# Optimization experiments

Measured on AMD Instinct MI355X. Metric: run time of the kernel, lower is better.

The kernel has to match this reference:

```python
import jax, jax.numpy as jnp
import numpy as np

DIM = 2048
HEADS = 16
DIM_HEAD = 128
DIM_INNER = HEADS * DIM_HEAD
BATCH = 2
SEQ = 2048
EPS = 1e-12  # F.normalize default eps


def l2norm(t, axis=-1):
    # matches F.normalize(t, dim=axis, p=2): t / max(||t||, eps)
    n = jnp.sqrt(jnp.sum(t * t, axis=axis, keepdims=True))
    return t / jnp.maximum(n, EPS)


def setup_inputs() -> dict:
    key = jax.random.key(0)
    ks = jax.random.split(key, 5)
    x = jax.random.normal(ks[0], (BATCH, SEQ, DIM), dtype=jnp.float32)
    # NormLinear weights (torch Linear layout: [out, in]); parametrization
    # l2-normalizes rows (dim=-1) for q/k/v and columns (dim=0) for to_out.
    Wq = jax.random.normal(ks[1], (DIM_INNER, DIM), dtype=jnp.float32) / np.sqrt(DIM)
    Wk = jax.random.normal(ks[2], (DIM_INNER, DIM), dtype=jnp.float32) / np.sqrt(DIM)
    Wv = jax.random.normal(ks[3], (DIM_INNER, DIM), dtype=jnp.float32) / np.sqrt(DIM)
    Wout = jax.random.normal(ks[4], (DIM, DIM_INNER), dtype=jnp.float32) / np.sqrt(DIM_INNER)
    # Scale(dim_inner, init=1.0, scale=dim**-1): param = ones * dim**-1,
    # forward_scale = init/scale = dim, so qk_scale() starts at 1.0
    qk_scale = jnp.ones((DIM_INNER,), dtype=jnp.float32) / DIM
    return {"x": x, "Wq": Wq, "Wk": Wk, "Wv": Wv, "Wout": Wout, "qk_scale": qk_scale}


def reference(x, Wq, Wk, Wv, Wout, qk_scale):
    b, n, _ = x.shape
    # NormLinear: x @ l2norm(W, rows).T  (scale = groups**-1 = 1)
    q = jnp.einsum('bnd,ed->bne', x, l2norm(Wq, axis=-1))
    k = jnp.einsum('bnd,ed->bne', x, l2norm(Wk, axis=-1))
    v = jnp.einsum('bnd,ed->bne', x, l2norm(Wv, axis=-1))
    # split heads: b n (h d) -> b h n d
    split = lambda t: t.reshape(b, n, HEADS, DIM_HEAD).transpose(0, 2, 1, 3)
    q, k, v = split(q), split(k), split(v)
    # per-head l2norm of q and k over head dim
    q = l2norm(q, axis=-1)
    k = l2norm(k, axis=-1)
    # learned qk scale: (h d) -> h 1 d, effective = param * forward_scale(=DIM)
    q = q * (qk_scale * DIM).reshape(HEADS, 1, DIM_HEAD)
    # causal SDPA with scale = sqrt(dim_head) (unit-norm q,k in nGPT)
    attn_scale = DIM_HEAD ** 0.5
    scores = jnp.einsum('bhid,bhjd->bhij', q, k) * attn_scale
    causal = jnp.tril(jnp.ones((n, n), dtype=bool))
    scores = jnp.where(causal, scores, jnp.finfo(scores.dtype).min)
    attn = jax.nn.softmax(scores, axis=-1)
    out = jnp.einsum('bhij,bhjd->bhid', attn, v)
    # merge heads: b h n d -> b n (h d)
    out = out.transpose(0, 2, 1, 3).reshape(b, n, DIM_INNER)
    # to_out: NormLinear with norm over dim=0 of weight [DIM, DIM_INNER]
    out = jnp.einsum('bne,de->bnd', out, l2norm(Wout, axis=0))
    return out
```

## Files before the change

### kernel.cpp

```cpp
#include <hip/hip_runtime.h>


typedef __bf16 bf16x8 __attribute__((ext_vector_type(8)));
typedef float f32x4 __attribute__((ext_vector_type(4)));

__device__ __forceinline__ unsigned short f2bf(float f) {
  unsigned int u = __float_as_uint(f);
  u = u + 0x7FFFu + ((u >> 16) & 1u);
  return (unsigned short)(u >> 16);
}

__device__ __forceinline__ void async16(const void* g, void* l) {
  __builtin_amdgcn_global_load_lds(
      (const __attribute__((address_space(1))) unsigned int*)g,
      (__attribute__((address_space(3))) unsigned int*)l, 16, 0, 0);
}

#define QFOLD (2048.0f * 11.313708498984761f * 1.4426950408889634f)


__global__ __launch_bounds__(256) void prep_w_rows(
    const float* __restrict__ Wq, const float* __restrict__ Wk,
    const float* __restrict__ Wv, ushort* __restrict__ oq,
    ushort* __restrict__ ok_, ushort* __restrict__ ov) {
  const int row = blockIdx.x;
  const float* W = (blockIdx.y == 0) ? Wq : (blockIdx.y == 1) ? Wk : Wv;
  ushort* O = (blockIdx.y == 0) ? oq : (blockIdx.y == 1) ? ok_ : ov;
  const int t = threadIdx.x;
  const float4* Wr = (const float4*)(W + (size_t)row * 2048);
  float4 v0 = Wr[t];
  float4 v1 = Wr[t + 256];
  float ss = v0.x * v0.x + v0.y * v0.y + v0.z * v0.z + v0.w * v0.w +
             v1.x * v1.x + v1.y * v1.y + v1.z * v1.z + v1.w * v1.w;
  ss += __shfl_xor(ss, 1);  ss += __shfl_xor(ss, 2);
  ss += __shfl_xor(ss, 4);  ss += __shfl_xor(ss, 8);
  ss += __shfl_xor(ss, 16); ss += __shfl_xor(ss, 32);
  __shared__ float red[4];
  if ((t & 63) == 0) red[t >> 6] = ss;
  __syncthreads();
  float tot = red[0] + red[1] + red[2] + red[3];
  float sc = 1.0f / fmaxf(sqrtf(tot), 1e-12f);
  ushort4 o0, o1;
  o0.x = f2bf(v0.x * sc); o0.y = f2bf(v0.y * sc);
  o0.z = f2bf(v0.z * sc); o0.w = f2bf(v0.w * sc);
  o1.x = f2bf(v1.x * sc); o1.y = f2bf(v1.y * sc);
  o1.z = f2bf(v1.z * sc); o1.w = f2bf(v1.w * sc);
  *(ushort4*)(O + (size_t)row * 2048 + t * 4) = o0;
  *(ushort4*)(O + (size_t)row * 2048 + 1024 + t * 4) = o1;
}

__global__ __launch_bounds__(256) void wout_colss(const float* __restrict__ W,
                                                  float* __restrict__ colss) {
  const int e = blockIdx.x * 256 + threadIdx.x;
  const int d0 = blockIdx.y * 128;
  float ss = 0.f;
  #pragma unroll 8
  for (int i = 0; i < 128; ++i) {
    float v = W[(size_t)(d0 + i) * 2048 + e];
    ss += v * v;
  }
  atomicAdd(colss + e, ss);
}

__global__ __launch_bounds__(256) void wout_norm(const float* __restrict__ W,
                                                 const float* __restrict__ colss,
                                                 ushort* __restrict__ O) {
  const int idx = (blockIdx.x * 256 + threadIdx.x) * 4;
  float4 v = *(const float4*)(W + idx);
  float4 c = *(const float4*)(colss + (idx & 2047));
  ushort4 o;
  o.x = f2bf(v.x / fmaxf(sqrtf(c.x), 1e-12f));
  o.y = f2bf(v.y / fmaxf(sqrtf(c.y), 1e-12f));
  o.z = f2bf(v.z / fmaxf(sqrtf(c.z), 1e-12f));
  o.w = f2bf(v.w / fmaxf(sqrtf(c.w), 1e-12f));
  *(ushort4*)(O + idx) = o;
}

__global__ __launch_bounds__(256) void convert_x(const float* __restrict__ X,
                                                 ushort* __restrict__ O) {
  const int idx = (blockIdx.x * 256 + threadIdx.x) * 4;
  float4 v = *(const float4*)(X + idx);
  ushort4 o;
  o.x = f2bf(v.x); o.y = f2bf(v.y); o.z = f2bf(v.z); o.w = f2bf(v.w);
  *(ushort4*)(O + idx) = o;
}

__global__ __launch_bounds__(64) void qk_mhead(const float* __restrict__ qks,
                                               float* __restrict__ mh) {
  const int h = blockIdx.x, l = threadIdx.x;
  float m = fmaxf(fabsf(qks[h * 128 + l]), fabsf(qks[h * 128 + 64 + l]));
  m = fmaxf(m, __shfl_xor(m, 1));  m = fmaxf(m, __shfl_xor(m, 2));
  m = fmaxf(m, __shfl_xor(m, 4));  m = fmaxf(m, __shfl_xor(m, 8));
  m = fmaxf(m, __shfl_xor(m, 16)); m = fmaxf(m, __shfl_xor(m, 32));
  if (l == 0) mh[h] = m * QFOLD;
}

__device__ __forceinline__ void gemm_mainloop(
    const ushort* __restrict__ A, const ushort* __restrict__ Bw,
    int m0, int n0, ushort* As, ushort* Bs, f32x4 acc[4][4],
    int t, int l, int wm, int wn) {
  const int l15 = l & 15, l4 = l >> 4;
  const ushort* abase = A + (size_t)m0 * 2048;
  const ushort* bbase = Bw + (size_t)n0 * 2048;
  for (int kt = 0; kt < 32; ++kt) {
    const int k0 = kt * 64;
    __syncthreads();
    #pragma unroll
    for (int p = 0; p < 9; ++p) {
      int c = p * 256 + t;
      const ushort* src = abase;
      char* dst = (char*)As;
      int cc = c;
      if (c >= 1152) { cc = c - 1152; src = bbase; dst = (char*)Bs; }
      int r = cc / 9, dc = cc - r * 9;
      int dcc = (dc == 8) ? 0 : dc;
      async16(src + (size_t)r * 2048 + k0 + dcc * 8, dst + cc * 16);
    }
    __syncthreads();
    #pragma unroll
    for (int ks = 0; ks < 2; ++ks) {
      bf16x8 af[4], bg[4];
      #pragma unroll
      for (int f = 0; f < 4; ++f)
        af[f] = *(const bf16x8*)&As[(wm * 64 + f * 16 + l15) * 72 + ks * 32 + l4 * 8];
      #pragma unroll
      for (int f = 0; f < 4; ++f)
        bg[f] = *(const bf16x8*)&Bs[(wn * 64 + f * 16 + l15) * 72 + ks * 32 + l4 * 8];
      #pragma unroll
      for (int fm = 0; fm < 4; ++fm)
        #pragma unroll
        for (int fn = 0; fn < 4; ++fn)
          acc[fm][fn] = __builtin_amdgcn_mfma_f32_16x16x32_bf16(
              af[fm], bg[fn], acc[fm][fn], 0, 0, 0);
    }
  }
}

__global__ __launch_bounds__(256, 4) void gemm_qkv(
    const ushort* __restrict__ X, const ushort* __restrict__ Wq,
    const ushort* __restrict__ Wk, const ushort* __restrict__ Wv,
    const float* __restrict__ qks, ushort* __restrict__ qn,
    ushort* __restrict__ kn, ushort* __restrict__ vt) {
  const int z = blockIdx.z;
  const ushort* Bw = (z == 0) ? Wq : (z == 1) ? Wk : Wv;
  const int n0 = blockIdx.x * 128;
  const int m0 = blockIdx.y * 128;
  __shared__ __align__(16) ushort As[128 * 72];
  __shared__ __align__(16) ushort Bs[128 * 72];
  __shared__ float partials[2][128];
  const int t = threadIdx.x, w = t >> 6, l = t & 63;
  const int wm = w & 1, wn = w >> 1;
  const int l15 = l & 15, l4 = l >> 4;

  f32x4 acc[4][4];
  #pragma unroll
  for (int i = 0; i < 4; ++i)
    #pragma unroll
    for (int j = 0; j < 4; ++j) acc[i][j] = (f32x4){0.f, 0.f, 0.f, 0.f};

  gemm_mainloop(X, Bw, m0, n0, As, Bs, acc, t, l, wm, wn);

  const int h = n0 >> 7;
  if (z == 2) {
    #pragma unroll
    for (int fm = 0; fm < 4; ++fm) {
      int mrow = m0 + wm * 64 + fm * 16 + l4 * 4;
      int bb = mrow >> 11;
      int nn = mrow & 2047;
      #pragma unroll
      for (int fn = 0; fn < 4; ++fn) {
        int d = wn * 64 + fn * 16 + l15;
        ushort4 p;
        p.x = f2bf(acc[fm][fn][0]); p.y = f2bf(acc[fm][fn][1]);
        p.z = f2bf(acc[fm][fn][2]); p.w = f2bf(acc[fm][fn][3]);
        *(ushort4*)(vt + (size_t)((bb * 16 + h) * 128 + d) * 2048 + nn) = p;
      }
    }
  } else {
    float rs[4][4];
    #pragma unroll
    for (int fm = 0; fm < 4; ++fm)
      #pragma unroll
      for (int r = 0; r < 4; ++r) {
        float s = 0.f;
        #pragma unroll
        for (int fn = 0; fn < 4; ++fn) {
          float v = acc[fm][fn][r];
          s += v * v;
        }
        s += __shfl_xor(s, 1); s += __shfl_xor(s, 2);
        s += __shfl_xor(s, 4); s += __shfl_xor(s, 8);
        rs[fm][r] = s;
      }
    if (l15 == 0) {
      #pragma unroll
      for (int fm = 0; fm < 4; ++fm)
        #pragma unroll
        for (int r = 0; r < 4; ++r)
          partials[wn][wm * 64 + fm * 16 + l4 * 4 + r] = rs[fm][r];
    }
    __syncthreads();
    float cs[4];
    #pragma unroll
    for (int fn = 0; fn < 4; ++fn)
      cs[fn] = (z == 0) ? qks[n0 + wn * 64 + fn * 16 + l15] * QFOLD : 1.0f;
    ushort* O = (z == 0) ? qn : kn;
    #pragma unroll
    for (int fm = 0; fm < 4; ++fm)
      #pragma unroll
      for (int r = 0; r < 4; ++r) {
        int i = wm * 64 + fm * 16 + l4 * 4 + r;
        float tot = partials[0][i] + partials[1][i];
        float sc = 1.0f / fmaxf(sqrtf(tot), 1e-12f);
        #pragma unroll
        for (int fn = 0; fn < 4; ++fn)
          O[(size_t)(m0 + i) * 2048 + n0 + wn * 64 + fn * 16 + l15] =
              f2bf(acc[fm][fn][r] * sc * cs[fn]);
      }
  }
}


#define LDSBUF 49152
#define ABYTES 32768

__device__ __forceinline__ void mainloop_256x128(
    const ushort* __restrict__ A, const ushort* __restrict__ Bw,
    int m0, int n0, char* lds, f32x4 acc[4][4], int t) {
  const int l = t & 63, w = t >> 6;
  const int wm = w & 3, wn = w >> 2;
  const int l15 = l & 15, l4 = l >> 4;

  const int lc = (t & 7) ^ ((t >> 3) & 7);
  const ushort* srcA = A + (size_t)m0 * 2048 + (t >> 3) * 2048 + lc * 8;
  const ushort* srcB = Bw + (size_t)n0 * 2048 + (t >> 3) * 2048 + lc * 8;
  char* dstA = lds + t * 16;
  char* dstB = lds + ABYTES + t * 16;

  const int rdA = (wm * 64 + l15) * 128;
  const int rdB = ABYTES + (wn * 64 + l15) * 128;
  const int cb0 = ((l4 ^ (l15 & 7)) * 16);
  const int cb1 = (((4 + l4) ^ (l15 & 7)) * 16);

  auto stageA = [&](int s, int k0, int o) {
    async16(srcA + (size_t)o * 131072 + k0, dstA + s * LDSBUF + o * 8192);
  };
  auto stageB = [&](int s, int k0, int o) {
    async16(srcB + (size_t)o * 131072 + k0, dstB + s * LDSBUF + o * 8192);
  };

  #pragma unroll
  for (int i = 0; i < 4; ++i)
    #pragma unroll
    for (int j = 0; j < 4; ++j) acc[i][j] = (f32x4){0.f, 0.f, 0.f, 0.f};

  stageA(0, 0, 0); stageA(0, 0, 1); stageA(0, 0, 2); stageA(0, 0, 3);
  stageB(0, 0, 0); stageB(0, 0, 1);
  stageA(1, 64, 0); stageA(1, 64, 1); stageA(1, 64, 2); stageA(1, 64, 3);
  stageB(1, 64, 0); stageB(1, 64, 1);
  asm volatile("s_waitcnt vmcnt(6)" ::: "memory");
  __builtin_amdgcn_s_barrier();

  auto tile = [&](int s, int s2, int k2, bool pf) {
    const char* Ab = lds + s * LDSBUF;
    bf16x8 af[4][2], bg[4][2];
    #pragma unroll
    for (int fm = 0; fm < 4; ++fm) {
      af[fm][0] = *(const bf16x8*)(Ab + rdA + fm * 2048 + cb0);
      af[fm][1] = *(const bf16x8*)(Ab + rdA + fm * 2048 + cb1);
    }
    #pragma unroll
    for (int fn = 0; fn < 2; ++fn) {
      bg[fn][0] = *(const bf16x8*)(Ab + rdB + fn * 2048 + cb0);
      bg[fn][1] = *(const bf16x8*)(Ab + rdB + fn * 2048 + cb1);
    }
    if (pf) { stageA(s2, k2, 0); stageA(s2, k2, 1); stageA(s2, k2, 2); }
    __builtin_amdgcn_s_setprio(1);
    #pragma unroll
    for (int ks = 0; ks < 2; ++ks)
      #pragma unroll
      for (int fm = 0; fm < 4; ++fm)
        #pragma unroll
        for (int fn = 0; fn < 2; ++fn)
          acc[fm][fn] = __builtin_amdgcn_mfma_f32_16x16x32_bf16(
              af[fm][ks], bg[fn][ks], acc[fm][fn], 0, 0, 0);
    __builtin_amdgcn_s_setprio(0);
    #pragma unroll
    for (int fn = 2; fn < 4; ++fn) {
      bg[fn][0] = *(const bf16x8*)(Ab + rdB + fn * 2048 + cb0);
      bg[fn][1] = *(const bf16x8*)(Ab + rdB + fn * 2048 + cb1);
    }
    if (pf) { stageA(s2, k2, 3); stageB(s2, k2, 0); stageB(s2, k2, 1); }
    __builtin_amdgcn_s_setprio(1);
    #pragma unroll
    for (int ks = 0; ks < 2; ++ks)
      #pragma unroll
      for (int fm = 0; fm < 4; ++fm)
        #pragma unroll
        for (int fn = 2; fn < 4; ++fn)
          acc[fm][fn] = __builtin_amdgcn_mfma_f32_16x16x32_bf16(
              af[fm][ks], bg[fn][ks], acc[fm][fn], 0, 0, 0);
    __builtin_amdgcn_s_setprio(0);
  };

  #pragma unroll 1
  for (int kt = 0; kt < 30; kt += 3) {
    tile(0, 2, (kt + 2) * 64, true);
    asm volatile("s_waitcnt vmcnt(6)" ::: "memory");
    __builtin_amdgcn_s_barrier();
    tile(1, 0, (kt + 3) * 64, true);
    asm volatile("s_waitcnt vmcnt(6)" ::: "memory");
    __builtin_amdgcn_s_barrier();
    tile(2, 1, (kt + 4) * 64, true);
    asm volatile("s_waitcnt vmcnt(6)" ::: "memory");
    __builtin_amdgcn_s_barrier();
  }
  tile(0, 0, 0, false);
  asm volatile("s_waitcnt vmcnt(0)" ::: "memory");
  __builtin_amdgcn_s_barrier();
  tile(1, 0, 0, false);
}

__global__ __launch_bounds__(256, 2) void attn_kernel(
    const ushort* __restrict__ qn, const ushort* __restrict__ kn,
    const ushort* __restrict__ vt, const float* __restrict__ mhead,
    ushort* __restrict__ ao) {
  const int hb = blockIdx.x;
  const int b = hb >> 4, h = hb & 15;
  const int y = blockIdx.y;
  const int qt = (y < 8) ? y : 23 - y;
  const int i0 = qt * 128;
  const int t = threadIdx.x, w = t >> 6, l = t & 63;
  const int l15 = l & 15, l4 = l >> 4;

  __shared__ __align__(16) ushort Ks[64 * 128];
  __shared__ __align__(16) ushort Vts[128 * 64];
  __shared__ __align__(16) ushort Ps[128 * 64];

  bf16x8 qf[2][4];
  #pragma unroll
  for (int fmq = 0; fmq < 2; ++fmq)
    #pragma unroll
    for (int ks = 0; ks < 4; ++ks)
      qf[fmq][ks] = *(const bf16x8*)(qn +
          (size_t)(b * 2048 + i0 + w * 32 + fmq * 16 + l15) * 2048 +
          h * 128 + ks * 32 + l4 * 8);

  f32x4 Oa[2][8];
  #pragma unroll
  for (int fmq = 0; fmq < 2; ++fmq)
    #pragma unroll
    for (int fd = 0; fd < 8; ++fd) Oa[fmq][fd] = (f32x4){0.f, 0.f, 0.f, 0.f};
  f32x4 Ol[2];
  Ol[0] = (f32x4){0.f, 0.f, 0.f, 0.f};
  Ol[1] = (f32x4){0.f, 0.f, 0.f, 0.f};

  const float mh = mhead[h];
  const __bf16 one = (__bf16)1.0f;
  const bf16x8 ones = {one, one, one, one, one, one, one, one};

  const ushort* kbase = kn + (size_t)(b * 2048) * 2048 + h * 128;
  const ushort* vbase = vt + (size_t)((b * 16 + h) * 128) * 2048;

  const int jtmax = 2 * qt + 1;
  for (int jt = 0; jt <= jtmax; ++jt) {
    const int j0 = jt * 64;
    __syncthreads();
    #pragma unroll
    for (int i = 0; i < 4; ++i) {
      int g = i * 256 + t;
      int r = g >> 4, pc = g & 15;
      async16(kbase + (size_t)(j0 + r) * 2048 + (pc ^ (r & 7)) * 8,
              (char*)Ks + g * 16);
    }
    #pragma unroll
    for (int i = 0; i < 4; ++i) {
      int g = i * 256 + t;
      int r = g >> 3, pc = g & 7;
      async16(vbase + (size_t)r * 2048 + j0 + (pc ^ (r & 7)) * 8,
              (char*)Vts + g * 16);
    }
    __syncthreads();

    f32x4 Sa[2][4];
    #pragma unroll
    for (int fj = 0; fj < 4; ++fj) {
      bf16x8 kf[4];
      #pragma unroll
      for (int ks = 0; ks < 4; ++ks)
        kf[ks] = *(const bf16x8*)&Ks[(fj * 16 + l15) * 128 +
                                     ((ks * 4 + l4) ^ (l15 & 7)) * 8];
      #pragma unroll
      for (int fmq = 0; fmq < 2; ++fmq) {
        f32x4 s0 = (f32x4){0.f, 0.f, 0.f, 0.f};
        #pragma unroll
        for (int ks = 0; ks < 4; ++ks)
          s0 = __builtin_amdgcn_mfma_f32_16x16x32_bf16(qf[fmq][ks], kf[ks],
                                                       s0, 0, 0, 0);
        Sa[fmq][fj] = s0;
      }
    }

    if (jt >= 2 * qt) {
      #pragma unroll
      for (int fmq = 0; fmq < 2; ++fmq)
        #pragma unroll
        for (int fj = 0; fj < 4; ++fj)
          #pragma unroll
          for (int r = 0; r < 4; ++r) {
            int jg = j0 + fj * 16 + l15;
            int ig = i0 + w * 32 + fmq * 16 + l4 * 4 + r;
            if (jg > ig) Sa[fmq][fj][r] = -1e30f;
          }
    }

    #pragma unroll
    for (int fmq = 0; fmq < 2; ++fmq)
      #pragma unroll
      for (int fj = 0; fj < 4; ++fj)
        #pragma unroll
        for (int r = 0; r < 4; ++r) {
          int qr = w * 32 + fmq * 16 + l4 * 4 + r;
          Ps[qr * 64 + ((fj * 16 + l15) ^ ((qr & 7) << 3))] =
              f2bf(__builtin_exp2f(Sa[fmq][fj][r] - mh));
        }

    #pragma unroll
    for (int ks = 0; ks < 2; ++ks) {
      bf16x8 p0[2];
      #pragma unroll
      for (int fmq = 0; fmq < 2; ++fmq) {
        int qr = w * 32 + fmq * 16 + l15;
        p0[fmq] = *(const bf16x8*)&Ps[qr * 64 +
                                      ((ks * 4 + l4) ^ (l15 & 7)) * 8];
        Ol[fmq] = __builtin_amdgcn_mfma_f32_16x16x32_bf16(p0[fmq], ones,
                                                          Ol[fmq], 0, 0, 0);
      }
      #pragma unroll
      for (int fd = 0; fd < 8; ++fd) {
        bf16x8 vf = *(const bf16x8*)&Vts[(fd * 16 + l15) * 64 +
                                         ((ks * 4 + l4) ^ (l15 & 7)) * 8];
        #pragma unroll
        for (int fmq = 0; fmq < 2; ++fmq)
          Oa[fmq][fd] = __builtin_amdgcn_mfma_f32_16x16x32_bf16(
              p0[fmq], vf, Oa[fmq][fd], 0, 0, 0);
      }
    }
  }

  #pragma unroll
  for (int fmq = 0; fmq < 2; ++fmq)
    #pragma unroll
    for (int r = 0; r < 4; ++r) {
      float inv = 1.0f / Ol[fmq][r];
      int ig = i0 + w * 32 + fmq * 16 + l4 * 4 + r;
      #pragma unroll
      for (int fd = 0; fd < 8; ++fd)
        ao[(size_t)(b * 2048 + ig) * 2048 + h * 128 + fd * 16 + l15] =
            f2bf(Oa[fmq][fd][r] * inv);
    }
}

__global__ __launch_bounds__(512, 2) void gemm_out(
    const ushort* __restrict__ A, const ushort* __restrict__ Bw,
    float* __restrict__ C) {
  __shared__ __align__(16) char lds[3 * LDSBUF];
  const int n0 = blockIdx.x * 128;
  const int m0 = blockIdx.y * 256;
  const int t = threadIdx.x;
  const int l = t & 63, w = t >> 6;
  const int wm = w & 3, wn = w >> 2;
  const int l15 = l & 15, l4 = l >> 4;

  f32x4 acc[4][4];
  mainloop_256x128(A, Bw, m0, n0, lds, acc, t);

  #pragma unroll
  for (int fm = 0; fm < 4; ++fm)
    #pragma unroll
    for (int fn = 0; fn < 4; ++fn)
      #pragma unroll
      for (int r = 0; r < 4; ++r)
        C[(size_t)(m0 + wm * 64 + fm * 16 + l4 * 4 + r) * 2048 +
          n0 + wn * 64 + fn * 16 + l15] = acc[fm][fn][r];
}

extern "C" void kernel_launch(void* const* d_in, const int* in_sizes, int n_in,
                              void* d_out, int out_size, void* d_ws, size_t ws_size,
                              hipStream_t stream) {
  (void)in_sizes; (void)n_in; (void)out_size; (void)ws_size;
  const float* x    = (const float*)d_in[0];
  const float* Wq   = (const float*)d_in[1];
  const float* Wk   = (const float*)d_in[2];
  const float* Wv   = (const float*)d_in[3];
  const float* Wout = (const float*)d_in[4];
  const float* qks  = (const float*)d_in[5];
  char* ws = (char*)d_ws;

  ushort* wqn  = (ushort*)(ws + 0);
  ushort* wkn  = (ushort*)(ws + 8388608);
  ushort* wvn  = (ushort*)(ws + 16777216);
  ushort* wotn = (ushort*)(ws + 25165824);
  ushort* xbf  = (ushort*)(ws + 33554432);
  ushort* qn   = (ushort*)(ws + 50331648);
  ushort* kn   = (ushort*)(ws + 67108864);
  ushort* vt   = (ushort*)(ws + 83886080);
  ushort* ao   = (ushort*)(ws + 100663296);
  float* colss = (float*)(ws + 117440512);
  float* mh    = (float*)(ws + 117448704);
  float* out   = (float*)d_out;

  hipMemsetAsync(colss, 0, 2048 * sizeof(float), stream);
  prep_w_rows<<<dim3(2048, 3), 256, 0, stream>>>(Wq, Wk, Wv, wqn, wkn, wvn);
  wout_colss<<<dim3(8, 16), 256, 0, stream>>>(Wout, colss);
  wout_norm<<<4096, 256, 0, stream>>>(Wout, colss, wotn);
  convert_x<<<8192, 256, 0, stream>>>(x, xbf);
  qk_mhead<<<16, 64, 0, stream>>>(qks, mh);
  gemm_qkv<<<dim3(16, 32, 3), 256, 0, stream>>>(xbf, wqn, wkn, wvn, qks, qn, kn, vt);
  attn_kernel<<<dim3(32, 16), 256, 0, stream>>>(qn, kn, vt, mh, ao);
  gemm_out<<<dim3(16, 16), 512, 0, stream>>>(ao, wotn, out);
}
```

Baseline: 384.0 us.

## Double-buffer K/V loads and pair causal query tiles per attention block

The attention kernel now prefetches the next K/V tile into a second LDS buffer while computing on the current one, replacing the load-then-compute pattern that needed two barriers per step. Each block also handles two query tiles (qt and 15-qt) one after the other, so every block does the same causal work, and the grid is halved to 256 blocks. LDS use grows to about 80KB per block, which may limit occupancy to one block per CU, and the halved grid leaves fewer blocks to hide latency.

```diff
diff --git a/kernel.cpp b/kernel.cpp
--- a/kernel.cpp
+++ b/kernel.cpp
@@ -328,32 +328,11 @@
   const int hb = blockIdx.x;
   const int b = hb >> 4, h = hb & 15;
   const int y = blockIdx.y;
-  const int qt = (y < 8) ? y : 23 - y;
-  const int i0 = qt * 128;
   const int t = threadIdx.x, w = t >> 6, l = t & 63;
   const int l15 = l & 15, l4 = l >> 4;
 
-  __shared__ __align__(16) ushort Ks[64 * 128];
-  __shared__ __align__(16) ushort Vts[128 * 64];
-  __shared__ __align__(16) ushort Ps[128 * 64];
-
-  bf16x8 qf[2][4];
-  #pragma unroll
-  for (int fmq = 0; fmq < 2; ++fmq)
-    #pragma unroll
-    for (int ks = 0; ks < 4; ++ks)
-      qf[fmq][ks] = *(const bf16x8*)(qn +
-          (size_t)(b * 2048 + i0 + w * 32 + fmq * 16 + l15) * 2048 +
-          h * 128 + ks * 32 + l4 * 8);
-
-  f32x4 Oa[2][8];
-  #pragma unroll
-  for (int fmq = 0; fmq < 2; ++fmq)
-    #pragma unroll
-    for (int fd = 0; fd < 8; ++fd) Oa[fmq][fd] = (f32x4){0.f, 0.f, 0.f, 0.f};
-  f32x4 Ol[2];
-  Ol[0] = (f32x4){0.f, 0.f, 0.f, 0.f};
-  Ol[1] = (f32x4){0.f, 0.f, 0.f, 0.f};
+  __shared__ __align__(16) char lds[2 * 32768 + 16384];
+  ushort* Ps = (ushort*)(lds + 65536);
 
   const float mh = mhead[h];
   const __bf16 one = (__bf16)1.0f;
@@ -362,103 +341,142 @@
   const ushort* kbase = kn + (size_t)(b * 2048) * 2048 + h * 128;
   const ushort* vbase = vt + (size_t)((b * 16 + h) * 128) * 2048;
 
-  const int jtmax = 2 * qt + 1;
-  for (int jt = 0; jt <= jtmax; ++jt) {
-    const int j0 = jt * 64;
-    __syncthreads();
+  auto stageKV = [&](int j0, int bufsel) {
+    char* kb = lds + bufsel * 32768;
+    char* vb = kb + 16384;
     #pragma unroll
     for (int i = 0; i < 4; ++i) {
       int g = i * 256 + t;
       int r = g >> 4, pc = g & 15;
-      async16(kbase + (size_t)(j0 + r) * 2048 + (pc ^ (r & 7)) * 8,
-              (char*)Ks + g * 16);
+      async16(kbase + (size_t)(j0 + r) * 2048 + (pc ^ (r & 7)) * 8, kb + g * 16);
     }
     #pragma unroll
     for (int i = 0; i < 4; ++i) {
       int g = i * 256 + t;
       int r = g >> 3, pc = g & 7;
-      async16(vbase + (size_t)r * 2048 + j0 + (pc ^ (r & 7)) * 8,
-              (char*)Vts + g * 16);
-    }
-    __syncthreads();
-
-    f32x4 Sa[2][4];
-    #pragma unroll
-    for (int fj = 0; fj < 4; ++fj) {
-      bf16x8 kf[4];
+      async16(vbase + (size_t)r * 2048 + j0 + (pc ^ (r & 7)) * 8, vb + g * 16);
+    }
+  };
+
+  #pragma unroll 1
+  for (int seg = 0; seg < 2; ++seg) {
+    const int qt = seg ? (15 - y) : y;
+    const int i0 = qt * 128;
+
+    bf16x8 qf[2][4];
+    #pragma unroll
+    for (int fmq = 0; fmq < 2; ++fmq)
       #pragma unroll
       for (int ks = 0; ks < 4; ++ks)
-        kf[ks] = *(const bf16x8*)&Ks[(fj * 16 + l15) * 128 +
-                                     ((ks * 4 + l4) ^ (l15 & 7)) * 8];
-      #pragma unroll
-      for (int fmq = 0; fmq < 2; ++fmq) {
-        f32x4 s0 = (f32x4){0.f, 0.f, 0.f, 0.f};
+        qf[fmq][ks] = *(const bf16x8*)(qn +
+            (size_t)(b * 2048 + i0 + w * 32 + fmq * 16 + l15) * 2048 +
+            h * 128 + ks * 32 + l4 * 8);
+
+    f32x4 Oa[2][8];
+    #pragma unroll
+    for (int fmq = 0; fmq < 2; ++fmq)
+      #pragma unroll
+      for (int fd = 0; fd < 8; ++fd) Oa[fmq][fd] = (f32x4){0.f, 0.f, 0.f, 0.f};
+    f32x4 Ol[2];
+    Ol[0] = (f32x4){0.f, 0.f, 0.f, 0.f};
+    Ol[1] = (f32x4){0.f, 0.f, 0.f, 0.f};
+
+    const int jtmax = 2 * qt + 1;
+
+    stageKV(0, 0);
+    asm volatile("s_waitcnt vmcnt(0)" ::: "memory");
+    __builtin_amdgcn_s_barrier();
+
+    #pragma unroll 1
+    for (int jt = 0; jt <= jtmax; ++jt) {
+      const int j0 = jt * 64;
+      const int buf = jt & 1;
+      if (jt < jtmax) stageKV(j0 + 64, buf ^ 1);
+
+      const ushort* Ks = (const ushort*)(lds + buf * 32768);
+      const ushort* Vts = (const ushort*)(lds + buf * 32768 + 16384);
+
+      f32x4 Sa[2][4];
+      #pragma unroll
+      for (int fj = 0; fj < 4; ++fj) {
+        bf16x8 kf[4];
         #pragma unroll
         for (int ks = 0; ks < 4; ++ks)
-          s0 = __builtin_amdgcn_mfma_f32_16x16x32_bf16(qf[fmq][ks], kf[ks],
-                                                       s0, 0, 0, 0);
-        Sa[fmq][fj] = s0;
-      }
-    }
-
-    if (jt >= 2 * qt) {
+          kf[ks] = *(const bf16x8*)&Ks[(fj * 16 + l15) * 128 +
+                                       ((ks * 4 + l4) ^ (l15 & 7)) * 8];
+        #pragma unroll
+        for (int fmq = 0; fmq < 2; ++fmq) {
+          f32x4 s0 = (f32x4){0.f, 0.f, 0.f, 0.f};
+          #pragma unroll
+          for (int ks = 0; ks < 4; ++ks)
+            s0 = __builtin_amdgcn_mfma_f32_16x16x32_bf16(qf[fmq][ks], kf[ks],
+                                                         s0, 0, 0, 0);
+          Sa[fmq][fj] = s0;
+        }
+      }
+
+      if (jt >= 2 * qt) {
+        #pragma unroll
+        for (int fmq = 0; fmq < 2; ++fmq)
+          #pragma unroll
+          for (int fj = 0; fj < 4; ++fj)
+            #pragma unroll
+            for (int r = 0; r < 4; ++r) {
+              int jg = j0 + fj * 16 + l15;
+              int ig = i0 + w * 32 + fmq * 16 + l4 * 4 + r;
+              if (jg > ig) Sa[fmq][fj][r] = -1e30f;
+            }
+      }
+
       #pragma unroll
       for (int fmq = 0; fmq < 2; ++fmq)
         #pragma unroll
         for (int fj = 0; fj < 4; ++fj)
           #pragma unroll
           for (int r = 0; r < 4; ++r) {
-            int jg = j0 + fj * 16 + l15;
-            int ig = i0 + w * 32 + fmq * 16 + l4 * 4 + r;
-            if (jg > ig) Sa[fmq][fj][r] = -1e30f;
+            int qr = w * 32 + fmq * 16 + l4 * 4 + r;
+            Ps[qr * 64 + ((fj * 16 + l15) ^ ((qr & 7) << 3))] =
+                f2bf(__builtin_exp2f(Sa[fmq][fj][r] - mh));
           }
+
+      #pragma unroll
+      for (int ks = 0; ks < 2; ++ks) {
+        bf16x8 p0[2];
+        #pragma unroll
+        for (int fmq = 0; fmq < 2; ++fmq) {
+          int qr = w * 32 + fmq * 16 + l15;
+          p0[fmq] = *(const bf16x8*)&Ps[qr * 64 +
+                                        ((ks * 4 + l4) ^ (l15 & 7)) * 8];
+          Ol[fmq] = __builtin_amdgcn_mfma_f32_16x16x32_bf16(p0[fmq], ones,
+                                                            Ol[fmq], 0, 0, 0);
+        }
+        #pragma unroll
+        for (int fd = 0; fd < 8; ++fd) {
+          bf16x8 vf = *(const bf16x8*)&Vts[(fd * 16 + l15) * 64 +
+                                           ((ks * 4 + l4) ^ (l15 & 7)) * 8];
+          #pragma unroll
+          for (int fmq = 0; fmq < 2; ++fmq)
+            Oa[fmq][fd] = __builtin_amdgcn_mfma_f32_16x16x32_bf16(
+                p0[fmq], vf, Oa[fmq][fd], 0, 0, 0);
+        }
+      }
+
+      asm volatile("s_waitcnt vmcnt(0)" ::: "memory");
+      __builtin_amdgcn_s_barrier();
     }
 
     #pragma unroll
     for (int fmq = 0; fmq < 2; ++fmq)
       #pragma unroll
-      for (int fj = 0; fj < 4; ++fj)
-        #pragma unroll
-        for (int r = 0; r < 4; ++r) {
-          int qr = w * 32 + fmq * 16 + l4 * 4 + r;
-          Ps[qr * 64 + ((fj * 16 + l15) ^ ((qr & 7) << 3))] =
-              f2bf(__builtin_exp2f(Sa[fmq][fj][r] - mh));
-        }
-
-    #pragma unroll
-    for (int ks = 0; ks < 2; ++ks) {
-      bf16x8 p0[2];
-      #pragma unroll
-      for (int fmq = 0; fmq < 2; ++fmq) {
-        int qr = w * 32 + fmq * 16 + l15;
-        p0[fmq] = *(const bf16x8*)&Ps[qr * 64 +
-                                      ((ks * 4 + l4) ^ (l15 & 7)) * 8];
-        Ol[fmq] = __builtin_amdgcn_mfma_f32_16x16x32_bf16(p0[fmq], ones,
-                                                          Ol[fmq], 0, 0, 0);
-      }
-      #pragma unroll
-      for (int fd = 0; fd < 8; ++fd) {
-        bf16x8 vf = *(const bf16x8*)&Vts[(fd * 16 + l15) * 64 +
-                                         ((ks * 4 + l4) ^ (l15 & 7)) * 8];
-        #pragma unroll
-        for (int fmq = 0; fmq < 2; ++fmq)
-          Oa[fmq][fd] = __builtin_amdgcn_mfma_f32_16x16x32_bf16(
-              p0[fmq], vf, Oa[fmq][fd], 0, 0, 0);
-      }
-    }
+      for (int r = 0; r < 4; ++r) {
+        float inv = 1.0f / Ol[fmq][r];
+        int ig = i0 + w * 32 + fmq * 16 + l4 * 4 + r;
+        #pragma unroll
+        for (int fd = 0; fd < 8; ++fd)
+          ao[(size_t)(b * 2048 + ig) * 2048 + h * 128 + fd * 16 + l15] =
+              f2bf(Oa[fmq][fd][r] * inv);
+      }
   }
-
-  #pragma unroll
-  for (int fmq = 0; fmq < 2; ++fmq)
-    #pragma unroll
-    for (int r = 0; r < 4; ++r) {
-      float inv = 1.0f / Ol[fmq][r];
-      int ig = i0 + w * 32 + fmq * 16 + l4 * 4 + r;
-      #pragma unroll
-      for (int fd = 0; fd < 8; ++fd)
-        ao[(size_t)(b * 2048 + ig) * 2048 + h * 128 + fd * 16 + l15] =
-            f2bf(Oa[fmq][fd][r] * inv);
-    }
 }
 
 __global__ __launch_bounds__(512, 2) void gemm_out(
@@ -517,6 +535,6 @@
   convert_x<<<8192, 256, 0, stream>>>(x, xbf);
   qk_mhead<<<16, 64, 0, stream>>>(qks, mh);
   gemm_qkv<<<dim3(16, 32, 3), 256, 0, stream>>>(xbf, wqn, wkn, wvn, qks, qn, kn, vt);
-  attn_kernel<<<dim3(32, 16), 256, 0, stream>>>(qn, kn, vt, mh, ao);
+  attn_kernel<<<dim3(32, 8), 256, 0, stream>>>(qn, kn, vt, mh, ao);
   gemm_out<<<dim3(16, 16), 512, 0, stream>>>(ao, wotn, out);
 }
```

Result: no change. 390.8 us (+1.8%).
